# Optimization experiments

Hardware: AMD Instinct MI355X
Metric: run time of the kernel (lower is better)

The kernel has to match this reference:

```python
import jax, jax.numpy as jnp
import numpy as np
import math

B, N, L, ED, H = 2, 32, 4, 64, 4   # graphs, nodes/graph, layers, embed_dim, heads
HD = ED // H
EPS = 1e-5


def _ln(x, g, b):
    m = x.mean(-1, keepdims=True)
    v = ((x - m) ** 2).mean(-1, keepdims=True)
    return (x - m) * jax.lax.rsqrt(v + EPS) * g + b


def _layer(x, W, b, lg, lb, fW, fb, fg, fbeta):
    # NOTE: in the torch source, ModuleList([Linear]*4) shares ONE linear for
    # q/k/v1/v2 and ONE LayerNorm for norms[0..2]; we reproduce that sharing.
    h = (x @ W.T + b).reshape(B, N, N, H, HD)
    q = _ln(h, lg, lb)                                    # q == k (shared LN)
    scores = jnp.einsum('bxahd,bayhd->bxayh', q, q) / math.sqrt(HD)
    att = jax.nn.softmax(scores, axis=2)                  # softmax over 'a'
    xu = jnp.einsum('bxahd,bayhd->bxayhd', h, h)          # v1 == v2 == h
    xu = _ln(xu, lg, lb)                                  # shared LN again
    xu = jnp.einsum('bxayh,bxayhd->bxyhd', att, xu).reshape(B, N, N, ED)
    y = jnp.concatenate([x, xu], axis=-1) @ fW.T + fb
    return _ln(y, fg, fbeta)


def _diag_offdiag_maxpool(x):
    # x: (B, ED, N, N)
    diag = jnp.diagonal(x, axis1=-2, axis2=-1)            # (B, ED, N)
    max_diag = diag.max(axis=2)                           # (B, ED)
    val = jnp.abs(max_diag.max() + (-x).max())
    eye = jnp.eye(N, dtype=x.dtype)
    max_offdiag = (x - val * eye).max(axis=(2, 3))        # (B, ED)
    return jnp.concatenate([max_diag, max_offdiag], axis=1)  # (B, 2*ED)


def setup_inputs() -> dict:
    key = jax.random.key(0)
    ks = jax.random.split(key, 12)
    E = 1024
    g = jax.random.randint(ks[0], (E,), 0, B)
    ls = jax.random.randint(ks[1], (E,), 0, N)
    ld = jax.random.randint(ks[2], (E,), 0, N)
    edge_index = jnp.stack([g * N + ls, g * N + ld]).astype(jnp.int64)
    batch = (jnp.arange(B * N) // N).astype(jnp.int64)
    std = 0.02
    return {
        'edge_index': edge_index,
        'batch': batch,
        'W0': jax.random.normal(ks[3], (ED, 1), jnp.float32) * std,
        'b0': jnp.zeros((ED,), jnp.float32),
        'Ws': jax.random.normal(ks[4], (L - 1, ED, ED), jnp.float32) * std,
        'bs': jnp.zeros((L - 1, ED), jnp.float32),
        'ln_g': jnp.ones((L, HD), jnp.float32),
        'ln_b': jnp.zeros((L, HD), jnp.float32),
        'fW0': jax.random.normal(ks[5], (ED, 1 + ED), jnp.float32) * std,
        'fb0': jnp.zeros((ED,), jnp.float32),
        'fWs': jax.random.normal(ks[6], (L - 1, ED, 2 * ED), jnp.float32) * std,
        'fbs': jnp.zeros((L - 1, ED), jnp.float32),
        'fln_g': jnp.ones((L, ED), jnp.float32),
        'fln_b': jnp.zeros((L, ED), jnp.float32),
        'opW': jax.random.normal(ks[7], (L, ED // 2, 2 * ED), jnp.float32) * std,
        'opb': jnp.zeros((L, ED // 2), jnp.float32),
    }


def reference(edge_index, batch, W0, b0, Ws, bs, ln_g, ln_b,
              fW0, fb0, fWs, fbs, fln_g, fln_b, opW, opb):
    # to_dense_adj with edge_attr = 1.0
    g = batch[edge_index[0]]
    ls = edge_index[0] - g * N
    ld = edge_index[1] - g * N
    adj = jnp.zeros((B, N, N), jnp.float32).at[g, ls, ld].add(1.0)
    idx = jnp.arange(N)
    adj = adj.at[:, idx, idx].set(2.0)
    x = adj[..., None]                                    # (B, N, N, 1)

    scores = jnp.zeros((B, ED // 2), jnp.float32)
    for i in range(L):
        W = W0 if i == 0 else Ws[i - 1]
        b = b0 if i == 0 else bs[i - 1]
        fW = fW0 if i == 0 else fWs[i - 1]
        fb = fb0 if i == 0 else fbs[i - 1]
        x = _layer(x, W, b, ln_g[i], ln_b[i], fW, fb, fln_g[i], fln_b[i])
        pooled = _diag_offdiag_maxpool(jnp.transpose(x, (0, 3, 1, 2)))
        scores = scores + pooled @ opW[i].T + opb[i]

    # BatchNorm1d(momentum=1.0, affine=False), training mode -> batch stats
    m = scores.mean(axis=0)
    v = scores.var(axis=0)
    return (scores - m) / jnp.sqrt(v + EPS)
```

## Files before the change

kernel.cpp:

```cpp
#include <hip/hip_runtime.h>
#include <math.h>

#define EPS 1e-5f

#define AG_LOAD(p)     __hip_atomic_load((p), __ATOMIC_RELAXED, __HIP_MEMORY_SCOPE_AGENT)
#define AG_STORE(p, v) __hip_atomic_store((p), (v), __ATOMIC_RELAXED, __HIP_MEMORY_SCOPE_AGENT)

struct Params {
    const int* ei; const int* batch; int E;
    const float* W0; const float* b0; const float* Ws; const float* bs;
    const float* ln_g; const float* ln_b;
    const float* fW0; const float* fb0; const float* fWs; const float* fbs;
    const float* fln_g; const float* fln_b;
    const float* opW; const float* opb;
    float* hA; float* qA;
    float* hB; float* qB;
    float* xbuf;
    float* Pmin; float* Poff; float* Pdg;
    int* bar;
    float* out;
};

__launch_bounds__(512, 1)
__global__ void k0(Params p) {
    const int tid  = threadIdx.x;
    const int blk  = blockIdx.x;
    const int gtid = blk * 512 + tid;
    const int c    = tid & 63;
    const int d    = c & 15;
    const int rl   = tid >> 6;
    const int r0     = blk * 8;
    const int b_blk  = r0 >> 10;
    const int xi_blk = (r0 >> 5) & 31;
    const int y0     = r0 & 31;
    const int rld    = xi_blk - y0;
    const int a_l  = c & 31;
    const int h1   = c >> 5;

    __shared__ float xslab[32];
    __shared__ float yslab[256];
    __shared__ __align__(16) float cA[64], cC[64], cW[64], cB0[64], cG[64], cBl[64];
    __shared__ float hstat[3][4];
    __shared__ __align__(16) float pp_s[256 * 68];
    __shared__ float A1_s[8 * 132];
    __shared__ float K0h_s[8][4];
    __shared__ __align__(16) float xrow[8][64];
    __shared__ __align__(16) float xu_s[8][64];
    __shared__ float Wf0[64];
    __shared__ __align__(16) float T65[64 * 68];
    __shared__ __align__(16) float ST[64 * 68];

    if (blk == 0 && tid == 0) p.bar[0] = 0;

    if (tid < 32)  xslab[tid] = 0.0f;
    if (tid < 256) yslab[tid] = 0.0f;

    if (tid < 64) {
        float Wc = p.W0[c], bc = p.b0[c];
        float sW = Wc, sB = bc;
        #pragma unroll
        for (int m = 1; m < 16; m <<= 1) {
            sW += __shfl_xor(sW, m, 16);
            sB += __shfl_xor(sB, m, 16);
        }
        float Ac = Wc - sW * 0.0625f;
        float Bc = bc - sB * 0.0625f;
        float sAA = Ac * Ac, sAB = Ac * Bc, sBB = Bc * Bc;
        #pragma unroll
        for (int m = 1; m < 16; m <<= 1) {
            sAA += __shfl_xor(sAA, m, 16);
            sAB += __shfl_xor(sAB, m, 16);
            sBB += __shfl_xor(sBB, m, 16);
        }
        cA[c] = Ac; cC[c] = Bc; cW[c] = Wc; cB0[c] = bc;
        cG[c] = p.ln_g[d]; cBl[c] = p.ln_b[d];
        if (d == 0) {
            hstat[0][c >> 4] = sAA * 0.0625f;
            hstat[1][c >> 4] = sAB * 0.0625f;
            hstat[2][c >> 4] = sBB * 0.0625f;
        }
        Wf0[tid] = p.fW0[tid * 65];
    }
    for (int i = tid; i < 1024; i += 512) {
        int cc = i >> 4, u = i & 15;
        const float* src = p.fW0 + cc * 65 + 1 + 4 * u;
        float4 w = make_float4(src[0], src[1], src[2], src[3]);
        *(float4*)(T65 + cc * 68 + 4 * ((u + 2 * cc) & 15)) = w;
    }
    for (int i = tid; i < 1024; i += 512) {
        float4 w = ((const float4*)p.Ws)[i];
        int cc = i >> 4, u = i & 15;
        *(float4*)(ST + cc * 68 + 4 * ((u + 2 * cc) & 15)) = w;
    }
    __syncthreads();

    for (int e2 = tid; e2 < p.E; e2 += 512) {
        int e0 = p.ei[e2], e1 = p.ei[p.E + e2];
        int g  = p.batch[e0];
        if (g == b_blk) {
            int ls = e0 - g * 32, ld = e1 - g * 32;
            if (ls == xi_blk) atomicAdd(&xslab[ld], 1.0f);
            unsigned dy = (unsigned)(ld - y0);
            if (dy < 8u) atomicAdd(&yslab[ls * 8 + dy], 1.0f);
        }
    }
    __syncthreads();
    if (tid == 0) xslab[xi_blk] = 2.0f;
    if (tid < 8)  yslab[(y0 + tid) * 8 + tid] = 2.0f;
    __syncthreads();

    const float vx = xslab[a_l];
    const float vy = yslab[a_l * 8 + rl];
    float s0, s1, is0, is1, w0m, w1m;
    {
        const int hh = h1;
        float rsx = rsqrtf(fmaf(fmaf(hstat[0][hh], vx, 2.0f * hstat[1][hh]), vx, hstat[2][hh]) + EPS);
        float rsy = rsqrtf(fmaf(fmaf(hstat[0][hh], vy, 2.0f * hstat[1][hh]), vy, hstat[2][hh]) + EPS);
        float qq = 0.f, sp = 0.f, sq = 0.f;
        #pragma unroll
        for (int t = 0; t < 4; ++t) {
            int dd = hh * 16 + 4 * t;
            float4 av = *(const float4*)(cA + dd);
            float4 bv = *(const float4*)(cC + dd);
            float4 wv = *(const float4*)(cW + dd);
            float4 b0v = *(const float4*)(cB0 + dd);
            float4 gv = *(const float4*)(cG + dd);
            float4 blv = *(const float4*)(cBl + dd);
            float4 ppv;
            float qx, qy;
            qx = fmaf(av.x, vx, bv.x) * rsx * gv.x + blv.x;
            qy = fmaf(av.x, vy, bv.x) * rsy * gv.x + blv.x;
            qq = fmaf(qx, qy, qq);
            ppv.x = fmaf(wv.x, vx, b0v.x) * fmaf(wv.x, vy, b0v.x);
            qx = fmaf(av.y, vx, bv.y) * rsx * gv.y + blv.y;
            qy = fmaf(av.y, vy, bv.y) * rsy * gv.y + blv.y;
            qq = fmaf(qx, qy, qq);
            ppv.y = fmaf(wv.y, vx, b0v.y) * fmaf(wv.y, vy, b0v.y);
            qx = fmaf(av.z, vx, bv.z) * rsx * gv.z + blv.z;
            qy = fmaf(av.z, vy, bv.z) * rsy * gv.z + blv.z;
            qq = fmaf(qx, qy, qq);
            ppv.z = fmaf(wv.z, vx, b0v.z) * fmaf(wv.z, vy, b0v.z);
            qx = fmaf(av.w, vx, bv.w) * rsx * gv.w + blv.w;
            qy = fmaf(av.w, vy, bv.w) * rsy * gv.w + blv.w;
            qq = fmaf(qx, qy, qq);
            ppv.w = fmaf(wv.w, vx, b0v.w) * fmaf(wv.w, vy, b0v.w);
            sp += ppv.x + ppv.y + ppv.z + ppv.w;
            sq += ppv.x*ppv.x + ppv.y*ppv.y + ppv.z*ppv.z + ppv.w*ppv.w;
            *(float4*)(pp_s + (a_l * 8 + rl) * 68 + 4 * (((hh * 4 + t) + 3 * a_l) & 15)) = ppv;
        }
        s0 = qq * 0.25f;
        float mu = sp * 0.0625f, var = fmaxf(sq * 0.0625f - mu * mu, 0.f);
        is0 = rsqrtf(var + EPS); w0m = mu * is0;
    }
    {
        const int hh = h1 + 2;
        float rsx = rsqrtf(fmaf(fmaf(hstat[0][hh], vx, 2.0f * hstat[1][hh]), vx, hstat[2][hh]) + EPS);
        float rsy = rsqrtf(fmaf(fmaf(hstat[0][hh], vy, 2.0f * hstat[1][hh]), vy, hstat[2][hh]) + EPS);
        float qq = 0.f, sp = 0.f, sq = 0.f;
        #pragma unroll
        for (int t = 0; t < 4; ++t) {
            int dd = hh * 16 + 4 * t;
            float4 av = *(const float4*)(cA + dd);
            float4 bv = *(const float4*)(cC + dd);
            float4 wv = *(const float4*)(cW + dd);
            float4 b0v = *(const float4*)(cB0 + dd);
            float4 gv = *(const float4*)(cG + dd);
            float4 blv = *(const float4*)(cBl + dd);
            float4 ppv;
            float qx, qy;
            qx = fmaf(av.x, vx, bv.x) * rsx * gv.x + blv.x;
            qy = fmaf(av.x, vy, bv.x) * rsy * gv.x + blv.x;
            qq = fmaf(qx, qy, qq);
            ppv.x = fmaf(wv.x, vx, b0v.x) * fmaf(wv.x, vy, b0v.x);
            qx = fmaf(av.y, vx, bv.y) * rsx * gv.y + blv.y;
            qy = fmaf(av.y, vy, bv.y) * rsy * gv.y + blv.y;
            qq = fmaf(qx, qy, qq);
            ppv.y = fmaf(wv.y, vx, b0v.y) * fmaf(wv.y, vy, b0v.y);
            qx = fmaf(av.z, vx, bv.z) * rsx * gv.z + blv.z;
            qy = fmaf(av.z, vy, bv.z) * rsy * gv.z + blv.z;
            qq = fmaf(qx, qy, qq);
            ppv.z = fmaf(wv.z, vx, b0v.z) * fmaf(wv.z, vy, b0v.z);
            qx = fmaf(av.w, vx, bv.w) * rsx * gv.w + blv.w;
            qy = fmaf(av.w, vy, bv.w) * rsy * gv.w + blv.w;
            qq = fmaf(qx, qy, qq);
            ppv.w = fmaf(wv.w, vx, b0v.w) * fmaf(wv.w, vy, b0v.w);
            sp += ppv.x + ppv.y + ppv.z + ppv.w;
            sq += ppv.x*ppv.x + ppv.y*ppv.y + ppv.z*ppv.z + ppv.w*ppv.w;
            *(float4*)(pp_s + (a_l * 8 + rl) * 68 + 4 * (((hh * 4 + t) + 3 * a_l) & 15)) = ppv;
        }
        s1 = qq * 0.25f;
        float mu = sp * 0.0625f, var = fmaxf(sq * 0.0625f - mu * mu, 0.f);
        is1 = rsqrtf(var + EPS); w1m = mu * is1;
    }

    float m0 = s0, m1 = s1;
    #pragma unroll
    for (int m = 1; m < 32; m <<= 1) {
        m0 = fmaxf(m0, __shfl_xor(m0, m));
        m1 = fmaxf(m1, __shfl_xor(m1, m));
    }
    float e0 = __expf(s0 - m0), e1 = __expf(s1 - m1);
    float l0 = e0, l1 = e1, k0a = e0 * w0m, k1a = e1 * w1m;
    #pragma unroll
    for (int m = 1; m < 32; m <<= 1) {
        l0 += __shfl_xor(l0, m);  l1 += __shfl_xor(l1, m);
        k0a += __shfl_xor(k0a, m); k1a += __shfl_xor(k1a, m);
    }
    A1_s[rl * 132 + h1 * 33 + a_l]       = e0 * is0 / l0;
    A1_s[rl * 132 + (h1 + 2) * 33 + a_l] = e1 * is1 / l1;
    if (a_l == 0) {
        K0h_s[rl][h1]     = k0a / l0;
        K0h_s[rl][h1 + 2] = k1a / l1;
    }

    {
        const int hc = c >> 4;
        float acc = 0.f;
        #pragma unroll
        for (int a = 0; a < 32; ++a) {
            float pv = pp_s[(a * 8 + rl) * 68 + 4 * (((c >> 2) + 3 * a) & 15) + (c & 3)];
            acc = fmaf(A1_s[rl * 132 + hc * 33 + a], pv, acc);
        }
        xu_s[rl][c] = (acc - K0h_s[rl][hc]) * cG[c] + cBl[c];
    }

    const float adjv = xslab[y0 + rl];
    float acc2 = fmaf(Wf0[c], adjv, p.fb0[c]);
    #pragma unroll
    for (int u = 0; u < 16; ++u) {
        float4 w = *(const float4*)(T65 + c * 68 + 4 * ((u + 2 * c) & 15));
        float4 xr = *(const float4*)(&xu_s[rl][4 * u]);
        acc2 = fmaf(w.x, xr.x, acc2); acc2 = fmaf(w.y, xr.y, acc2);
        acc2 = fmaf(w.z, xr.z, acc2); acc2 = fmaf(w.w, xr.w, acc2);
    }
    float t1 = acc2;
    #pragma unroll
    for (int m = 1; m < 64; m <<= 1) t1 += __shfl_xor(t1, m, 64);
    float mu = t1 * (1.0f / 64.0f);
    float dv2 = acc2 - mu;
    float t2 = dv2 * dv2;
    #pragma unroll
    for (int m = 1; m < 64; m <<= 1) t2 += __shfl_xor(t2, m, 64);
    float xnew = dv2 * rsqrtf(t2 * (1.0f / 64.0f) + EPS) * p.fln_g[c] + p.fln_b[c];
    xrow[rl][c]  = xnew;
    p.xbuf[gtid] = xnew;
    __syncthreads();

    if (tid < 64) {
        float mn = 1e30f, off = -1e30f, dg = -1e30f;
        #pragma unroll
        for (int r2 = 0; r2 < 8; ++r2) {
            float v = xrow[r2][tid];
            mn = fminf(mn, v);
            if (r2 == rld) dg = v; else off = fmaxf(off, v);
        }
        int o = blk * 64 + tid;
        p.Pmin[o] = mn; p.Poff[o] = off; p.Pdg[o] = dg;
    }

    {
        float acc = p.bs[c];
        #pragma unroll
        for (int u = 0; u < 16; ++u) {
            float4 w = *(const float4*)(ST + c * 68 + 4 * ((u + 2 * c) & 15));
            float4 xr = *(const float4*)(&xrow[rl][4 * u]);
            acc = fmaf(w.x, xr.x, acc); acc = fmaf(w.y, xr.y, acc);
            acc = fmaf(w.z, xr.z, acc); acc = fmaf(w.w, xr.w, acc);
        }
        p.hA[gtid] = acc;
    }
}

__launch_bounds__(512, 1)
__global__ void klayer(Params p, int layer, int is_last) {
    const int tid  = threadIdx.x;
    const int blk  = blockIdx.x;
    const int gtid = blk * 512 + tid;
    const int c    = tid & 63;
    const int d    = c & 15;
    const int rl   = tid >> 6;
    const int r0     = blk * 8;
    const int b_blk  = r0 >> 10;
    const int xi_blk = (r0 >> 5) & 31;
    const int y0     = r0 & 31;
    const int rld    = xi_blk - y0;
    const int slab_off = (b_blk * 1024 + xi_blk * 32) * 64;
    const int a_l  = c & 31;
    const int h1   = c >> 5;

    const float* hin = (layer == 2) ? p.hB : p.hA;
    float* hout = (layer == 1) ? p.hB : p.hA;

    __shared__ __align__(16) float hx_s[32 * 68];
    __shared__ __align__(16) float pp_s[256 * 68];
    __shared__ float A1_s[8 * 132];
    __shared__ float K0h_s[8][4];
    __shared__ __align__(16) float xrow[8][64];
    __shared__ __align__(16) float xu_s[8][64];
    __shared__ __align__(16) float FT[64 * 132];
    __shared__ __align__(16) float ST[64 * 68];
    __shared__ __align__(16) float g16[16], b16[16];
    __shared__ float vals[4];
    __shared__ float scores_s[64];
    __shared__ int tailflag;
    float* sm_mn  = pp_s;
    float* sm_off = pp_s + 512;
    float* sm_dg  = pp_s + 1024;
    float* psum   = pp_s + 1536;

    float xv = p.xbuf[gtid];
    float4 hsl = ((const float4*)(hin + slab_off))[tid];
    const float* hyp = hin + (b_blk * 1024 + a_l * 32 + y0 + rl) * 64;
    float4 hvA[4], hvB[4];
    #pragma unroll
    for (int t = 0; t < 4; ++t) {
        hvA[t] = *(const float4*)(hyp + h1 * 16 + 4 * t);
        hvB[t] = *(const float4*)(hyp + (h1 + 2) * 16 + 4 * t);
    }

    if (tid < 16) {
        g16[tid] = p.ln_g[layer * 16 + tid];
        b16[tid] = p.ln_b[layer * 16 + tid];
    }

    {
        int a = tid >> 4, t = tid & 15, pr = (t + 2 * a) & 15;
        *(float4*)(hx_s + a * 68 + 4 * pr) = hsl;
    }
    {
        const float* fw = p.fWs + (layer - 1) * 8192;
        for (int i = tid; i < 2048; i += 512) {
            float4 w = ((const float4*)fw)[i];
            int cc = i >> 5, u = i & 31;
            *(float4*)(FT + cc * 132 + 4 * ((u + 2 * cc) & 31)) = w;
        }
    }
    if (!is_last) {
        const float* sw = p.Ws + layer * 4096;
        for (int i = tid; i < 1024; i += 512) {
            float4 w = ((const float4*)sw)[i];
            int cc = i >> 4, u = i & 15;
            *(float4*)(ST + cc * 68 + 4 * ((u + 2 * cc) & 15)) = w;
        }
    }
    xrow[rl][c] = xv;
    __syncthreads();

    float s0, s1, is0, is1, w0m, w1m;
    {
        const int hh = h1;
        float4 xh4[4];
        float sxp = 0.f, sxq = 0.f, syp = 0.f, syq = 0.f;
        #pragma unroll
        for (int t = 0; t < 4; ++t) {
            float4 v = *(const float4*)(hx_s + a_l * 68 + 4 * (((hh * 4 + t) + 2 * a_l) & 15));
            xh4[t] = v;
            sxp += v.x + v.y + v.z + v.w;
            sxq += v.x*v.x + v.y*v.y + v.z*v.z + v.w*v.w;
            float4 y = hvA[t];
            syp += y.x + y.y + y.z + y.w;
            syq += y.x*y.x + y.y*y.y + y.z*y.z + y.w*y.w;
        }
        float mxm = sxp * 0.0625f;
        float rsx = rsqrtf(fmaxf(sxq * 0.0625f - mxm * mxm, 0.f) + EPS);
        float mym = syp * 0.0625f;
        float rsy = rsqrtf(fmaxf(syq * 0.0625f - mym * mym, 0.f) + EPS);
        float qq = 0.f, sp = 0.f, sq = 0.f;
        #pragma unroll
        for (int t = 0; t < 4; ++t) {
            float4 g4 = *(const float4*)(g16 + 4 * t);
            float4 b4 = *(const float4*)(b16 + 4 * t);
            float4 xh = xh4[t], yh = hvA[t];
            float4 ppv;
            float qx, qy;
            qx = (xh.x - mxm) * rsx * g4.x + b4.x;
            qy = (yh.x - mym) * rsy * g4.x + b4.x;
            qq = fmaf(qx, qy, qq);  ppv.x = xh.x * yh.x;
            qx = (xh.y - mxm) * rsx * g4.y + b4.y;
            qy = (yh.y - mym) * rsy * g4.y + b4.y;
            qq = fmaf(qx, qy, qq);  ppv.y = xh.y * yh.y;
            qx = (xh.z - mxm) * rsx * g4.z + b4.z;
            qy = (yh.z - mym) * rsy * g4.z + b4.z;
            qq = fmaf(qx, qy, qq);  ppv.z = xh.z * yh.z;
            qx = (xh.w - mxm) * rsx * g4.w + b4.w;
            qy = (yh.w - mym) * rsy * g4.w + b4.w;
            qq = fmaf(qx, qy, qq);  ppv.w = xh.w * yh.w;
            sp += ppv.x + ppv.y + ppv.z + ppv.w;
            sq += ppv.x*ppv.x + ppv.y*ppv.y + ppv.z*ppv.z + ppv.w*ppv.w;
            *(float4*)(pp_s + (a_l * 8 + rl) * 68 + 4 * (((hh * 4 + t) + 3 * a_l) & 15)) = ppv;
        }
        s0 = qq * 0.25f;
        float mu = sp * 0.0625f, var = fmaxf(sq * 0.0625f - mu * mu, 0.f);
        is0 = rsqrtf(var + EPS); w0m = mu * is0;
    }
    {
        const int hh = h1 + 2;
        float4 xh4[4];
        float sxp = 0.f, sxq = 0.f, syp = 0.f, syq = 0.f;
        #pragma unroll
        for (int t = 0; t < 4; ++t) {
            float4 v = *(const float4*)(hx_s + a_l * 68 + 4 * (((hh * 4 + t) + 2 * a_l) & 15));
            xh4[t] = v;
            sxp += v.x + v.y + v.z + v.w;
            sxq += v.x*v.x + v.y*v.y + v.z*v.z + v.w*v.w;
            float4 y = hvB[t];
            syp += y.x + y.y + y.z + y.w;
            syq += y.x*y.x + y.y*y.y + y.z*y.z + y.w*y.w;
        }
        float mxm = sxp * 0.0625f;
        float rsx = rsqrtf(fmaxf(sxq * 0.0625f - mxm * mxm, 0.f) + EPS);
        float mym = syp * 0.0625f;
        float rsy = rsqrtf(fmaxf(syq * 0.0625f - mym * mym, 0.f) + EPS);
        float qq = 0.f, sp = 0.f, sq = 0.f;
        #pragma unroll
        for (int t = 0; t < 4; ++t) {
            float4 g4 = *(const float4*)(g16 + 4 * t);
            float4 b4 = *(const float4*)(b16 + 4 * t);
            float4 xh = xh4[t], yh = hvB[t];
            float4 ppv;
            float qx, qy;
            qx = (xh.x - mxm) * rsx * g4.x + b4.x;
            qy = (yh.x - mym) * rsy * g4.x + b4.x;
            qq = fmaf(qx, qy, qq);  ppv.x = xh.x * yh.x;
            qx = (xh.y - mxm) * rsx * g4.y + b4.y;
            qy = (yh.y - mym) * rsy * g4.y + b4.y;
            qq = fmaf(qx, qy, qq);  ppv.y = xh.y * yh.y;
            qx = (xh.z - mxm) * rsx * g4.z + b4.z;
            qy = (yh.z - mym) * rsy * g4.z + b4.z;
            qq = fmaf(qx, qy, qq);  ppv.z = xh.z * yh.z;
            qx = (xh.w - mxm) * rsx * g4.w + b4.w;
            qy = (yh.w - mym) * rsy * g4.w + b4.w;
            qq = fmaf(qx, qy, qq);  ppv.w = xh.w * yh.w;
            sp += ppv.x + ppv.y + ppv.z + ppv.w;
            sq += ppv.x*ppv.x + ppv.y*ppv.y + ppv.z*ppv.z + ppv.w*ppv.w;
            *(float4*)(pp_s + (a_l * 8 + rl) * 68 + 4 * (((hh * 4 + t) + 3 * a_l) & 15)) = ppv;
        }
        s1 = qq * 0.25f;
        float mu = sp * 0.0625f, var = fmaxf(sq * 0.0625f - mu * mu, 0.f);
        is1 = rsqrtf(var + EPS); w1m = mu * is1;
    }

    float m0 = s0, m1 = s1;
    #pragma unroll
    for (int m = 1; m < 32; m <<= 1) {
        m0 = fmaxf(m0, __shfl_xor(m0, m));
        m1 = fmaxf(m1, __shfl_xor(m1, m));
    }
    float e0 = __expf(s0 - m0), e1 = __expf(s1 - m1);
    float l0 = e0, l1 = e1, k0a = e0 * w0m, k1a = e1 * w1m;
    #pragma unroll
    for (int m = 1; m < 32; m <<= 1) {
        l0 += __shfl_xor(l0, m);  l1 += __shfl_xor(l1, m);
        k0a += __shfl_xor(k0a, m); k1a += __shfl_xor(k1a, m);
    }
    A1_s[rl * 132 + h1 * 33 + a_l]       = e0 * is0 / l0;
    A1_s[rl * 132 + (h1 + 2) * 33 + a_l] = e1 * is1 / l1;
    if (a_l == 0) {
        K0h_s[rl][h1]     = k0a / l0;
        K0h_s[rl][h1 + 2] = k1a / l1;
    }

    {
        const int hc = c >> 4;
        float acc = 0.f;
        #pragma unroll
        for (int a = 0; a < 32; ++a) {
            float pv = pp_s[(a * 8 + rl) * 68 + 4 * (((c >> 2) + 3 * a) & 15) + (c & 3)];
            acc = fmaf(A1_s[rl * 132 + hc * 33 + a], pv, acc);
        }
        xu_s[rl][c] = (acc - K0h_s[rl][hc]) * g16[d] + b16[d];
    }

    float acc2 = p.fbs[(layer - 1) * 64 + c];
    #pragma unroll
    for (int u = 0; u < 16; ++u) {
        float4 w = *(const float4*)(FT + c * 132 + 4 * ((u + 2 * c) & 31));
        float4 xr = *(const float4*)(&xrow[rl][4 * u]);
        acc2 = fmaf(w.x, xr.x, acc2); acc2 = fmaf(w.y, xr.y, acc2);
        acc2 = fmaf(w.z, xr.z, acc2); acc2 = fmaf(w.w, xr.w, acc2);
    }
    #pragma unroll
    for (int u = 16; u < 32; ++u) {
        float4 w = *(const float4*)(FT + c * 132 + 4 * ((u + 2 * c) & 31));
        float4 xr = *(const float4*)(&xu_s[rl][4 * (u - 16)]);
        acc2 = fmaf(w.x, xr.x, acc2); acc2 = fmaf(w.y, xr.y, acc2);
        acc2 = fmaf(w.z, xr.z, acc2); acc2 = fmaf(w.w, xr.w, acc2);
    }
    float t1 = acc2;
    #pragma unroll
    for (int m = 1; m < 64; m <<= 1) t1 += __shfl_xor(t1, m, 64);
    float mu = t1 * (1.0f / 64.0f);
    float dv2 = acc2 - mu;
    float t2 = dv2 * dv2;
    #pragma unroll
    for (int m = 1; m < 64; m <<= 1) t2 += __shfl_xor(t2, m, 64);
    float xnew = dv2 * rsqrtf(t2 * (1.0f / 64.0f) + EPS) *
                 p.fln_g[layer * 64 + c] + p.fln_b[layer * 64 + c];
    __syncthreads();
    xrow[rl][c] = xnew;
    if (!is_last) p.xbuf[gtid] = xnew;
    __syncthreads();

    if (tid < 64) {
        float mn = 1e30f, off = -1e30f, dg = -1e30f;
        #pragma unroll
        for (int r2 = 0; r2 < 8; ++r2) {
            float v = xrow[r2][tid];
            mn = fminf(mn, v);
            if (r2 == rld) dg = v; else off = fmaxf(off, v);
        }
        int o = layer * 16384 + blk * 64 + tid;
        if (is_last) {
            AG_STORE(&p.Pmin[o], mn); AG_STORE(&p.Poff[o], off); AG_STORE(&p.Pdg[o], dg);
        } else {
            p.Pmin[o] = mn; p.Poff[o] = off; p.Pdg[o] = dg;
        }
    }

    if (!is_last) {
        float acc = p.bs[layer * 64 + c];
        #pragma unroll
        for (int u = 0; u < 16; ++u) {
            float4 w = *(const float4*)(ST + c * 68 + 4 * ((u + 2 * c) & 15));
            float4 xr = *(const float4*)(&xrow[rl][4 * u]);
            acc = fmaf(w.x, xr.x, acc); acc = fmaf(w.y, xr.y, acc);
            acc = fmaf(w.z, xr.z, acc); acc = fmaf(w.w, xr.w, acc);
        }
        hout[gtid] = acc;
        return;
    }

    __syncthreads();
    if (tid == 0) {
        int r = __hip_atomic_fetch_add(p.bar, 1, __ATOMIC_RELAXED,
                                       __HIP_MEMORY_SCOPE_AGENT);
        tailflag = (r == 255) ? 1 : 0;
    }
    __syncthreads();
    if (!tailflag) return;

    {
        int l = tid >> 7, bb = (tid >> 6) & 1, e = tid & 63;
        float mn = 1e30f, off = -1e30f, dg = -1e30f;
        #pragma unroll 4
        for (int k = 0; k < 128; ++k) {
            int o = l * 16384 + (bb * 128 + k) * 64 + e;
            float vmn, voff, vdg;
            if (l == 3) { vmn = AG_LOAD(&p.Pmin[o]); voff = AG_LOAD(&p.Poff[o]); vdg = AG_LOAD(&p.Pdg[o]); }
            else        { vmn = p.Pmin[o];           voff = p.Poff[o];           vdg = p.Pdg[o]; }
            mn  = fminf(mn,  vmn);
            off = fmaxf(off, voff);
            dg  = fmaxf(dg,  vdg);
        }
        sm_mn[tid] = mn; sm_off[tid] = off; sm_dg[tid] = dg;
    }
    __syncthreads();
    if (tid < 4) {
        float gmx = -1e30f, gmn = 1e30f;
        for (int i2 = 0; i2 < 128; ++i2) {
            gmx = fmaxf(gmx, sm_dg[tid * 128 + i2]);
            gmn = fminf(gmn, sm_mn[tid * 128 + i2]);
        }
        vals[tid] = fabsf(gmx - gmn);
    }
    __syncthreads();
    {
        int bb = tid >> 8, cc = (tid >> 3) & 31, pp = tid & 7;
        float a2 = 0.0f;
        for (int l = 0; l < 4; ++l) {
            float val = vals[l];
            const float* Wr = p.opW + l * 4096 + cc * 128;
            int base = l * 128 + bb * 64;
            for (int j = pp * 16; j < pp * 16 + 16; ++j) {
                float pv;
                if (j < 64) pv = sm_dg[base + j];
                else        pv = fmaxf(sm_off[base + j - 64], sm_dg[base + j - 64] - val);
                a2 = fmaf(Wr[j], pv, a2);
            }
        }
        psum[tid] = a2;
    }
    __syncthreads();
    if (tid < 64) {
        int bb = tid >> 5, cc = tid & 31;
        float a2 = 0.0f;
        for (int l = 0; l < 4; ++l) a2 += p.opb[l * 32 + cc];
        for (int pp = 0; pp < 8; ++pp) a2 += psum[bb * 256 + cc * 8 + pp];
        scores_s[tid] = a2;
    }
    __syncthreads();
    if (tid < 32) {
        float sA = scores_s[tid], sB = scores_s[32 + tid];
        float mu2 = 0.5f * (sA + sB);
        float va = 0.5f * ((sA - mu2) * (sA - mu2) + (sB - mu2) * (sB - mu2));
        float inv = rsqrtf(va + EPS);
        p.out[tid]      = (sA - mu2) * inv;
        p.out[32 + tid] = (sB - mu2) * inv;
    }
}

extern "C" void kernel_launch(void* const* d_in, const int* in_sizes, int n_in,
                              void* d_out, int out_size, void* d_ws, size_t ws_size,
                              hipStream_t stream) {
    Params prm;
    prm.ei    = (const int*)d_in[0];
    prm.batch = (const int*)d_in[1];
    prm.E     = in_sizes[0] / 2;
    prm.W0    = (const float*)d_in[2];
    prm.b0    = (const float*)d_in[3];
    prm.Ws    = (const float*)d_in[4];
    prm.bs    = (const float*)d_in[5];
    prm.ln_g  = (const float*)d_in[6];
    prm.ln_b  = (const float*)d_in[7];
    prm.fW0   = (const float*)d_in[8];
    prm.fb0   = (const float*)d_in[9];
    prm.fWs   = (const float*)d_in[10];
    prm.fbs   = (const float*)d_in[11];
    prm.fln_g = (const float*)d_in[12];
    prm.fln_b = (const float*)d_in[13];
    prm.opW   = (const float*)d_in[14];
    prm.opb   = (const float*)d_in[15];

    float* ws = (float*)d_ws;
    prm.hA    = ws;
    prm.qA    = prm.hA   + 131072;
    prm.hB    = prm.qA   + 131072;
    prm.qB    = prm.hB   + 131072;
    prm.xbuf  = prm.qB   + 131072;
    prm.Pmin  = prm.xbuf + 131072;
    prm.Poff  = prm.Pmin + 65536;
    prm.Pdg   = prm.Poff + 65536;
    prm.bar   = (int*)(prm.Pdg + 65536);
    prm.out   = (float*)d_out;

    k0<<<256, 512, 0, stream>>>(prm);
    klayer<<<256, 512, 0, stream>>>(prm, 1, 0);
    klayer<<<256, 512, 0, stream>>>(prm, 2, 0);
    klayer<<<256, 512, 0, stream>>>(prm, 3, 1);
}
```

Measured before the change: 158.8 us.

## Store transposed h copy for contiguous y-slab loads and recompute products on the fly

Each producing kernel now writes h a second time in transposed (b, y, x, c) order. The consumer layer can then load its 8-row y-slab as one contiguous coalesced block into shared memory, instead of strided per-thread float4 gathers. The pp_s product buffer is removed, and hx*hy products are recomputed from shared memory inside the attention-weighted sum. This costs an extra global write per layer and extra multiplies in the inner loop.

```diff
diff --git a/kernel.cpp b/kernel.cpp
--- a/kernel.cpp
+++ b/kernel.cpp
@@ -13,8 +13,8 @@
     const float* fW0; const float* fb0; const float* fWs; const float* fbs;
     const float* fln_g; const float* fln_b;
     const float* opW; const float* opb;
-    float* hA; float* qA;
-    float* hB; float* qB;
+    float* hA; float* hAT;
+    float* hB; float* hBT;
     float* xbuf;
     float* Pmin; float* Poff; float* Pdg;
     int* bar;
@@ -268,6 +268,7 @@
             acc = fmaf(w.z, xr.z, acc); acc = fmaf(w.w, xr.w, acc);
         }
         p.hA[gtid] = acc;
+        p.hAT[((b_blk * 32 + y0 + rl) * 32 + xi_blk) * 64 + c] = acc;
     }
 }
 
@@ -288,11 +289,13 @@
     const int a_l  = c & 31;
     const int h1   = c >> 5;
 
-    const float* hin = (layer == 2) ? p.hB : p.hA;
-    float* hout = (layer == 1) ? p.hB : p.hA;
+    const float* hin  = (layer == 2) ? p.hB  : p.hA;
+    const float* hinT = (layer == 2) ? p.hBT : p.hAT;
+    float* hout  = (layer == 1) ? p.hB  : p.hA;
+    float* houtT = (layer == 1) ? p.hBT : p.hAT;
 
     __shared__ __align__(16) float hx_s[32 * 68];
-    __shared__ __align__(16) float pp_s[256 * 68];
+    __shared__ __align__(16) float yT_s[256 * 68];
     __shared__ float A1_s[8 * 132];
     __shared__ float K0h_s[8][4];
     __shared__ __align__(16) float xrow[8][64];
@@ -303,29 +306,30 @@
     __shared__ float vals[4];
     __shared__ float scores_s[64];
     __shared__ int tailflag;
-    float* sm_mn  = pp_s;
-    float* sm_off = pp_s + 512;
-    float* sm_dg  = pp_s + 1024;
-    float* psum   = pp_s + 1536;
+    float* sm_mn  = yT_s;
+    float* sm_off = yT_s + 512;
+    float* sm_dg  = yT_s + 1024;
+    float* psum   = yT_s + 1536;
 
     float xv = p.xbuf[gtid];
-    float4 hsl = ((const float4*)(hin + slab_off))[tid];
-    const float* hyp = hin + (b_blk * 1024 + a_l * 32 + y0 + rl) * 64;
-    float4 hvA[4], hvB[4];
-    #pragma unroll
-    for (int t = 0; t < 4; ++t) {
-        hvA[t] = *(const float4*)(hyp + h1 * 16 + 4 * t);
-        hvB[t] = *(const float4*)(hyp + (h1 + 2) * 16 + 4 * t);
-    }
-
+    {
+        const float4* src = (const float4*)(hinT + (b_blk * 32 + y0) * 2048);
+        #pragma unroll
+        for (int k = 0; k < 8; ++k) {
+            int i = tid + k * 512;
+            float4 v = src[i];
+            int rl2 = i >> 9, a = (i >> 4) & 31, u = i & 15;
+            *(float4*)(yT_s + (rl2 * 32 + a) * 68 + 4 * ((u + 2 * a) & 15)) = v;
+        }
+    }
+    {
+        float4 hsl = ((const float4*)(hin + slab_off))[tid];
+        int a = tid >> 4, t = tid & 15, pr = (t + 2 * a) & 15;
+        *(float4*)(hx_s + a * 68 + 4 * pr) = hsl;
+    }
     if (tid < 16) {
         g16[tid] = p.ln_g[layer * 16 + tid];
         b16[tid] = p.ln_b[layer * 16 + tid];
-    }
-
-    {
-        int a = tid >> 4, t = tid & 15, pr = (t + 2 * a) & 15;
-        *(float4*)(hx_s + a * 68 + 4 * pr) = hsl;
     }
     {
         const float* fw = p.fWs + (layer - 1) * 8192;
@@ -349,15 +353,16 @@
     float s0, s1, is0, is1, w0m, w1m;
     {
         const int hh = h1;
-        float4 xh4[4];
+        float4 xh4[4], yh4[4];
         float sxp = 0.f, sxq = 0.f, syp = 0.f, syq = 0.f;
         #pragma unroll
         for (int t = 0; t < 4; ++t) {
-            float4 v = *(const float4*)(hx_s + a_l * 68 + 4 * (((hh * 4 + t) + 2 * a_l) & 15));
-            xh4[t] = v;
+            int ps = 4 * (((hh * 4 + t) + 2 * a_l) & 15);
+            float4 v = *(const float4*)(hx_s + a_l * 68 + ps);
+            float4 y = *(const float4*)(yT_s + (rl * 32 + a_l) * 68 + ps);
+            xh4[t] = v; yh4[t] = y;
             sxp += v.x + v.y + v.z + v.w;
             sxq += v.x*v.x + v.y*v.y + v.z*v.z + v.w*v.w;
-            float4 y = hvA[t];
             syp += y.x + y.y + y.z + y.w;
             syq += y.x*y.x + y.y*y.y + y.z*y.z + y.w*y.w;
         }
@@ -370,7 +375,7 @@
         for (int t = 0; t < 4; ++t) {
             float4 g4 = *(const float4*)(g16 + 4 * t);
             float4 b4 = *(const float4*)(b16 + 4 * t);
-            float4 xh = xh4[t], yh = hvA[t];
+            float4 xh = xh4[t], yh = yh4[t];
             float4 ppv;
             float qx, qy;
             qx = (xh.x - mxm) * rsx * g4.x + b4.x;
@@ -387,7 +392,6 @@
             qq = fmaf(qx, qy, qq);  ppv.w = xh.w * yh.w;
             sp += ppv.x + ppv.y + ppv.z + ppv.w;
             sq += ppv.x*ppv.x + ppv.y*ppv.y + ppv.z*ppv.z + ppv.w*ppv.w;
-            *(float4*)(pp_s + (a_l * 8 + rl) * 68 + 4 * (((hh * 4 + t) + 3 * a_l) & 15)) = ppv;
         }
         s0 = qq * 0.25f;
         float mu = sp * 0.0625f, var = fmaxf(sq * 0.0625f - mu * mu, 0.f);
@@ -395,15 +399,16 @@
     }
     {
         const int hh = h1 + 2;
-        float4 xh4[4];
+        float4 xh4[4], yh4[4];
         float sxp = 0.f, sxq = 0.f, syp = 0.f, syq = 0.f;
         #pragma unroll
         for (int t = 0; t < 4; ++t) {
-            float4 v = *(const float4*)(hx_s + a_l * 68 + 4 * (((hh * 4 + t) + 2 * a_l) & 15));
-            xh4[t] = v;
+            int ps = 4 * (((hh * 4 + t) + 2 * a_l) & 15);
+            float4 v = *(const float4*)(hx_s + a_l * 68 + ps);
+            float4 y = *(const float4*)(yT_s + (rl * 32 + a_l) * 68 + ps);
+            xh4[t] = v; yh4[t] = y;
             sxp += v.x + v.y + v.z + v.w;
             sxq += v.x*v.x + v.y*v.y + v.z*v.z + v.w*v.w;
-            float4 y = hvB[t];
             syp += y.x + y.y + y.z + y.w;
             syq += y.x*y.x + y.y*y.y + y.z*y.z + y.w*y.w;
         }
@@ -416,7 +421,7 @@
         for (int t = 0; t < 4; ++t) {
             float4 g4 = *(const float4*)(g16 + 4 * t);
             float4 b4 = *(const float4*)(b16 + 4 * t);
-            float4 xh = xh4[t], yh = hvB[t];
+            float4 xh = xh4[t], yh = yh4[t];
             float4 ppv;
             float qx, qy;
             qx = (xh.x - mxm) * rsx * g4.x + b4.x;
@@ -433,7 +438,6 @@
             qq = fmaf(qx, qy, qq);  ppv.w = xh.w * yh.w;
             sp += ppv.x + ppv.y + ppv.z + ppv.w;
             sq += ppv.x*ppv.x + ppv.y*ppv.y + ppv.z*ppv.z + ppv.w*ppv.w;
-            *(float4*)(pp_s + (a_l * 8 + rl) * 68 + 4 * (((hh * 4 + t) + 3 * a_l) & 15)) = ppv;
         }
         s1 = qq * 0.25f;
         float mu = sp * 0.0625f, var = fmaxf(sq * 0.0625f - mu * mu, 0.f);
@@ -462,11 +466,14 @@
 
     {
         const int hc = c >> 4;
+        const int ce = c & 3;
         float acc = 0.f;
         #pragma unroll
         for (int a = 0; a < 32; ++a) {
-            float pv = pp_s[(a * 8 + rl) * 68 + 4 * (((c >> 2) + 3 * a) & 15) + (c & 3)];
-            acc = fmaf(A1_s[rl * 132 + hc * 33 + a], pv, acc);
+            int ps = 4 * (((c >> 2) + 2 * a) & 15) + ce;
+            float hxv = hx_s[a * 68 + ps];
+            float hyv = yT_s[(rl * 32 + a) * 68 + ps];
+            acc = fmaf(A1_s[rl * 132 + hc * 33 + a], hxv * hyv, acc);
         }
         xu_s[rl][c] = (acc - K0h_s[rl][hc]) * g16[d] + b16[d];
     }
@@ -527,6 +534,7 @@
             acc = fmaf(w.z, xr.z, acc); acc = fmaf(w.w, xr.w, acc);
         }
         hout[gtid] = acc;
+        houtT[((b_blk * 32 + y0 + rl) * 32 + xi_blk) * 64 + c] = acc;
         return;
     }
 
@@ -623,10 +631,10 @@
 
     float* ws = (float*)d_ws;
     prm.hA    = ws;
-    prm.qA    = prm.hA   + 131072;
-    prm.hB    = prm.qA   + 131072;
-    prm.qB    = prm.hB   + 131072;
-    prm.xbuf  = prm.qB   + 131072;
+    prm.hAT   = prm.hA   + 131072;
+    prm.hB    = prm.hAT  + 131072;
+    prm.hBT   = prm.hB   + 131072;
+    prm.xbuf  = prm.hBT  + 131072;
     prm.Pmin  = prm.xbuf + 131072;
     prm.Poff  = prm.Pmin + 65536;
     prm.Pdg   = prm.Poff + 65536;
```

Measured after the change: 157.5 us, median of 2. No clear change (-0.8%).
